# Performance work log

Measured on AMD Instinct MI355X. Metric: run time of the kernel, lower is better.

Reference implementation:

```python
import jax, jax.numpy as jnp
import numpy as np

# dims
C = 16      # input_channels
H = 64      # hidden_channels
HID = 128   # CDEFunc hidden width (hardcoded in source)
OUT = 1     # output_channels
L = 128     # number of time knots -> L-1 spline segments
B = 2048    # batch


def setup_inputs() -> dict:
    key = jax.random.key(0)
    ks = jax.random.split(key, 9)
    n = lambda k, shape, s: (jax.random.normal(k, shape, dtype=jnp.float32) * s)
    return {
        # cubic Hermite spline coeffs: concat(a, b, two_c, three_d) along last dim
        "coeffs": n(ks[0], (B, L - 1, 4 * C), 0.1),
        "W_init": n(ks[1], (H, C), 0.2),
        "b_init": jnp.zeros((H,), jnp.float32),
        "W1": n(ks[2], (HID, H), 0.1),
        "b1": jnp.zeros((HID,), jnp.float32),
        "W2": n(ks[3], (H * C, HID), 0.05),
        "b2": jnp.zeros((H * C,), jnp.float32),
        "W_out": n(ks[4], (OUT, H), 0.1),
        "b_out": jnp.zeros((OUT,), jnp.float32),
    }


def _spline_deriv(coeffs, t):
    """dX/dt of cubic spline at scalar time t. coeffs: (B, L-1, 4C)."""
    idx = jnp.clip(jnp.floor(t).astype(jnp.int32), 0, L - 2)
    seg = jax.lax.dynamic_slice_in_dim(coeffs, idx, 1, axis=1)[:, 0]  # (B, 4C)
    a, b, two_c, three_d = jnp.split(seg, 4, axis=-1)
    fr = t - idx.astype(t.dtype) if hasattr(t, 'dtype') else t - idx
    return b + two_c * fr + three_d * (fr * fr)  # (B, C)


def reference(coeffs, W_init, b_init, W1, b1, W2, b2, W_out, b_out):
    # X(0) = a of first segment (frac = 0)
    X0 = coeffs[:, 0, :C]
    z0 = X0 @ W_init.T + b_init  # (B, H)

    def f(z, dX):
        # CDEFunc: linear-relu-linear-tanh -> (B, H, C), then contract with dX/dt
        h = jax.nn.relu(z @ W1.T + b1)
        g = jnp.tanh(h @ W2.T + b2).reshape(-1, H, C)
        return jnp.einsum('bhc,bc->bh', g, dX)

    dt = jnp.float32(1.0)  # one RK4 step per knot interval

    def step(z, t):
        d0 = _spline_deriv(coeffs, t)
        dm = _spline_deriv(coeffs, t + 0.5 * dt)
        d1 = _spline_deriv(coeffs, t + dt)
        k1 = f(z, d0)
        k2 = f(z + 0.5 * dt * k1, dm)
        k3 = f(z + 0.5 * dt * k2, dm)
        k4 = f(z + dt * k3, d1)
        return z + (dt / 6.0) * (k1 + 2.0 * k2 + 2.0 * k3 + k4), None

    ts = jnp.arange(L - 1, dtype=jnp.float32)
    zT, _ = jax.lax.scan(step, z0, ts)
    return zT @ W_out.T + b_out  # (B, OUT)
```

## Files before the change

kernel.cpp:

```cpp
#include <hip/hip_runtime.h>

#define L_DIM 128
#define BB 8

typedef _Float16 f16;
typedef _Float16 f16x8 __attribute__((ext_vector_type(8)));
typedef float f32x4 __attribute__((ext_vector_type(4)));

__device__ __forceinline__ float fast_tanh_b(float x, float bk) {
    float e = __builtin_amdgcn_exp2f(fmaf(x, 2.8853900817779268f, bk));
    float r = __builtin_amdgcn_rcpf(e + 1.0f);
    return fmaf(-2.0f, r, 1.0f);
}

__attribute__((amdgpu_flat_work_group_size(512, 512), amdgpu_waves_per_eu(2)))
__global__ void
cde_kernel(const float* __restrict__ coeffs,
           const float* __restrict__ W_init, const float* __restrict__ b_init,
           const float* __restrict__ W1, const float* __restrict__ b1,
           const float* __restrict__ W2, const float* __restrict__ b2,
           const float* __restrict__ W_out, const float* __restrict__ b_out,
           float* __restrict__ out)
{
    __shared__ __align__(16) f16   z16[16][72];
    __shared__ __align__(16) f16   h16[16][136];
    __shared__ __align__(16) float dxT[2][3][16][20];
    __shared__ __align__(16) float zf[BB][64];

    const int tid  = threadIdx.x;
    const int blk  = blockIdx.x;
    const int lane = tid & 63;
    const int w    = tid >> 6;
    const int q    = lane >> 4;
    const int lr   = lane & 15;
    const int hh   = w * 8 + (lr & 7);
    const int chp  = lr >> 3;
    const int row0 = (q & 1) * 4 + (q >> 1) * 2;

    f16x8 w2f[8][4];
    float b2k[8];
#pragma unroll
    for (int t8 = 0; t8 < 8; ++t8) {
        const int outc = hh * 16 + 2 * t8 + chp;
        b2k[t8] = 2.8853900817779268f * b2[outc];
#pragma unroll
        for (int kc = 0; kc < 4; ++kc) {
            const float* src = W2 + (size_t)outc * 128 + kc * 32 + q * 8;
            f16x8 v;
#pragma unroll
            for (int i = 0; i < 8; ++i) v[i] = (f16)src[i];
            w2f[t8][kc] = v;
        }
    }
    f16x8 w1f[2];
#pragma unroll
    for (int kc = 0; kc < 2; ++kc) {
        const float* src = W1 + (size_t)(w * 16 + lr) * 64 + kc * 32 + q * 8;
        f16x8 v;
#pragma unroll
        for (int i = 0; i < 8; ++i) v[i] = (f16)src[i];
        w1f[kc] = v;
    }
    const float b1r = b1[w * 16 + lr];
    const f32x4 zero4 = {0.f, 0.f, 0.f, 0.f};

    float z32r[2], ksumr[2];
#pragma unroll
    for (int j = 0; j < 2; ++j) {
        const float* x0 = coeffs + (size_t)(blk * BB + row0 + j) * (L_DIM - 1) * 64;
        float a = b_init[hh];
#pragma unroll
        for (int c = 0; c < 16; ++c) a = fmaf(x0[c], W_init[hh * 16 + c], a);
        z32r[j] = a;
        ksumr[j] = 0.f;
        if (lr < 8) z16[row0 + j][hh] = (f16)a;
    }
    for (int i = tid; i < 8 * 72; i += 512) z16[8 + i / 72][i % 72] = (f16)0.f;
    if (tid < BB * 16) {
        const int b = tid >> 4, c = tid & 15;
        const float* seg = coeffs + (size_t)(blk * BB + b) * (L_DIM - 1) * 64;
        float bv = seg[16 + c], cv = seg[32 + c], dv = seg[48 + c];
        dxT[0][0][c][b] = bv;
        dxT[0][1][c][b] = fmaf(0.25f, dv, fmaf(0.5f, cv, bv));
        dxT[0][2][c][b] = seg[64 + 16 + c];
    }
    __syncthreads();

#define G2TILE(dst, T) \
    f32x4 dst = __builtin_amdgcn_mfma_f32_16x16x32_f16(af0, w2f[T][0], zero4, 0, 0, 0); \
    dst = __builtin_amdgcn_mfma_f32_16x16x32_f16(af1, w2f[T][1], dst, 0, 0, 0);         \
    dst = __builtin_amdgcn_mfma_f32_16x16x32_f16(af2, w2f[T][2], dst, 0, 0, 0);         \
    dst = __builtin_amdgcn_mfma_f32_16x16x32_f16(af3, w2f[T][3], dst, 0, 0, 0);

#define G2TAIL(src, T) {                                                  \
    float u0 = __shfl_xor(src[2], 32);                                    \
    float u1 = __shfl_xor(src[3], 32);                                    \
    float g0 = fast_tanh_b((lane < 32) ? src[0] : u0, b2k[T]);            \
    float g1 = fast_tanh_b((lane < 32) ? src[1] : u1, b2k[T]);            \
    ka0 = fmaf(g0, dvv[(T) & 3].x, ka0);                                  \
    ka1 = fmaf(g1, dvv[(T) & 3].y, ka1); }

    for (int t = 0; t < L_DIM - 1; ++t) {
        const int buf = t & 1;
        float pb = 0.f, pc = 0.f, pd = 0.f, pe = 0.f;
#pragma unroll
        for (int s = 0; s < 4; ++s) {
            {
                f16x8 za0 = *(const f16x8*)&z16[lr][q * 8];
                f16x8 za1 = *(const f16x8*)&z16[lr][32 + q * 8];
                f32x4 hacc = __builtin_amdgcn_mfma_f32_16x16x32_f16(za0, w1f[0], zero4, 0, 0, 0);
                hacc = __builtin_amdgcn_mfma_f32_16x16x32_f16(za1, w1f[1], hacc, 0, 0, 0);
#pragma unroll
                for (int r = 0; r < 4; ++r)
                    h16[q * 4 + r][w * 16 + lr] = (f16)fmaxf(hacc[r] + b1r, 0.f);
            }
            __syncthreads();

            const int ds = (s + 1) >> 1;
            float ka0 = 0.f, ka1 = 0.f;
#pragma unroll
            for (int hf = 0; hf < 2; ++hf) {
                float2 dvv[4];
#pragma unroll
                for (int tt = 0; tt < 4; ++tt)
                    dvv[tt] = *(const float2*)&dxT[buf][ds][2 * (hf * 4 + tt) + chp][row0];
                const f16x8 af0 = *(const f16x8*)&h16[lr][q * 8];
                const f16x8 af1 = *(const f16x8*)&h16[lr][32 + q * 8];
                const f16x8 af2 = *(const f16x8*)&h16[lr][64 + q * 8];
                const f16x8 af3 = *(const f16x8*)&h16[lr][96 + q * 8];
                G2TILE(a0, hf * 4 + 0)
                G2TILE(a1, hf * 4 + 1)
                G2TAIL(a0, hf * 4 + 0)
                G2TILE(a2, hf * 4 + 2)
                G2TAIL(a1, hf * 4 + 1)
                G2TILE(a3, hf * 4 + 3)
                if (hf == 0 && s == 2 && t < L_DIM - 2 && tid < 128) {
                    const int b = tid >> 4, c = tid & 15;
                    const float* seg = coeffs + ((size_t)(blk * BB + b) * (L_DIM - 1) + (t + 1)) * 64;
                    pb = seg[16 + c]; pc = seg[32 + c]; pd = seg[48 + c];
                    pe = (t + 1 < L_DIM - 2) ? seg[80 + c] : 0.f;
                }
                G2TAIL(a2, hf * 4 + 2)
                G2TAIL(a3, hf * 4 + 3)
            }
            ka0 += __shfl_xor(ka0, 8);
            ka1 += __shfl_xor(ka1, 8);
            float zs0, zs1;
            if (s == 3) {
                z32r[0] = fmaf(ksumr[0] + ka0, 1.f / 6.f, z32r[0]); zs0 = z32r[0];
                z32r[1] = fmaf(ksumr[1] + ka1, 1.f / 6.f, z32r[1]); zs1 = z32r[1];
            } else {
                ksumr[0] = (s == 0) ? ka0 : fmaf(2.f, ka0, ksumr[0]);
                ksumr[1] = (s == 0) ? ka1 : fmaf(2.f, ka1, ksumr[1]);
                const float alpha = (s == 2) ? 1.f : 0.5f;
                zs0 = fmaf(alpha, ka0, z32r[0]);
                zs1 = fmaf(alpha, ka1, z32r[1]);
            }
            if (lr < 8) {
                z16[row0 + 0][hh] = (f16)zs0;
                z16[row0 + 1][hh] = (f16)zs1;
            }
            if (s == 3 && t < L_DIM - 2 && tid < 128) {
                const int b = tid >> 4, c = tid & 15;
                dxT[buf ^ 1][0][c][b] = pb;
                dxT[buf ^ 1][1][c][b] = fmaf(0.25f, pd, fmaf(0.5f, pc, pb));
                dxT[buf ^ 1][2][c][b] = (t + 1 < L_DIM - 2) ? pe : (pb + pc + pd);
            }
            __syncthreads();
        }
    }

    if (lr < 8) {
        zf[row0 + 0][hh] = z32r[0];
        zf[row0 + 1][hh] = z32r[1];
    }
    __syncthreads();
    if (tid < 64) {
        const int b = lane >> 3, j0 = lane & 7;
        float p = 0.f;
#pragma unroll
        for (int m = 0; m < 8; ++m) p += zf[b][j0 + 8 * m] * W_out[j0 + 8 * m];
        p += __shfl_xor(p, 1, 64);
        p += __shfl_xor(p, 2, 64);
        p += __shfl_xor(p, 4, 64);
        if (j0 == 0) out[blk * BB + b] = p + b_out[0];
    }
}

extern "C" void kernel_launch(void* const* d_in, const int* in_sizes, int n_in,
                              void* d_out, int out_size, void* d_ws, size_t ws_size,
                              hipStream_t stream) {
    const float* coeffs = (const float*)d_in[0];
    const float* W_init = (const float*)d_in[1];
    const float* b_init = (const float*)d_in[2];
    const float* W1     = (const float*)d_in[3];
    const float* b1     = (const float*)d_in[4];
    const float* W2     = (const float*)d_in[5];
    const float* b2     = (const float*)d_in[6];
    const float* W_out  = (const float*)d_in[7];
    const float* b_out  = (const float*)d_in[8];
    cde_kernel<<<256, 512, 0, stream>>>(coeffs, W_init, b_init, W1, b1, W2, b2,
                                        W_out, b_out, (float*)d_out);
}
```

Before: 662.4 us.

## Preload all spline derivatives into LDS and vectorize hidden-layer store

All spline derivative values for every time step (start and midpoint) are computed and staged into shared memory before the time loop. This replaces the per-step double-buffered global prefetch and its extra writes inside the loop. The first MFMA's operands are swapped so each lane writes four consecutive hidden outputs as one f16x4 store with a float4 bias load, instead of four scalar stores. The cost is about 130KB of LDS per block and a longer prologue.

Result: no change. 666.5 us (+0.6%).

```diff
diff --git a/kernel.cpp b/kernel.cpp
--- a/kernel.cpp
+++ b/kernel.cpp
@@ -4,6 +4,7 @@
 #define BB 8
 
 typedef _Float16 f16;
+typedef _Float16 f16x4 __attribute__((ext_vector_type(4)));
 typedef _Float16 f16x8 __attribute__((ext_vector_type(8)));
 typedef float f32x4 __attribute__((ext_vector_type(4)));
 
@@ -24,8 +25,9 @@
 {
     __shared__ __align__(16) f16   z16[16][72];
     __shared__ __align__(16) f16   h16[16][136];
-    __shared__ __align__(16) float dxT[2][3][16][20];
     __shared__ __align__(16) float zf[BB][64];
+    __shared__ __align__(16) float dxb[128][16][8];
+    __shared__ __align__(16) float dxm[127][16][8];
 
     const int tid  = threadIdx.x;
     const int blk  = blockIdx.x;
@@ -61,7 +63,7 @@
         for (int i = 0; i < 8; ++i) v[i] = (f16)src[i];
         w1f[kc] = v;
     }
-    const float b1r = b1[w * 16 + lr];
+    const float4 b1q = *(const float4*)&b1[w * 16 + q * 4];
     const f32x4 zero4 = {0.f, 0.f, 0.f, 0.f};
 
     float z32r[2], ksumr[2];
@@ -76,22 +78,24 @@
         if (lr < 8) z16[row0 + j][hh] = (f16)a;
     }
     for (int i = tid; i < 8 * 72; i += 512) z16[8 + i / 72][i % 72] = (f16)0.f;
-    if (tid < BB * 16) {
-        const int b = tid >> 4, c = tid & 15;
-        const float* seg = coeffs + (size_t)(blk * BB + b) * (L_DIM - 1) * 64;
-        float bv = seg[16 + c], cv = seg[32 + c], dv = seg[48 + c];
-        dxT[0][0][c][b] = bv;
-        dxT[0][1][c][b] = fmaf(0.25f, dv, fmaf(0.5f, cv, bv));
-        dxT[0][2][c][b] = seg[64 + 16 + c];
+
+#pragma unroll 2
+    for (int i = tid; i < 127 * 128; i += 512) {
+        const int t = i >> 7, j = i & 127;
+        const int c = j & 15, b = (j >> 4) & 7;
+        const float* seg = coeffs + ((size_t)(blk * BB + b) * (L_DIM - 1) + t) * 64;
+        const float bv = seg[16 + c], cv = seg[32 + c], dv = seg[48 + c];
+        dxb[t][c][b] = bv;
+        dxm[t][c][b] = fmaf(0.25f, dv, fmaf(0.5f, cv, bv));
+        if (t == 126) dxb[127][c][b] = bv + cv + dv;
     }
     __syncthreads();
 
-#define G2TILE(dst, T) \
+#define G2T(dst, T) \
     f32x4 dst = __builtin_amdgcn_mfma_f32_16x16x32_f16(af0, w2f[T][0], zero4, 0, 0, 0); \
     dst = __builtin_amdgcn_mfma_f32_16x16x32_f16(af1, w2f[T][1], dst, 0, 0, 0);         \
     dst = __builtin_amdgcn_mfma_f32_16x16x32_f16(af2, w2f[T][2], dst, 0, 0, 0);         \
     dst = __builtin_amdgcn_mfma_f32_16x16x32_f16(af3, w2f[T][3], dst, 0, 0, 0);
-
 #define G2TAIL(src, T) {                                                  \
     float u0 = __shfl_xor(src[2], 32);                                    \
     float u1 = __shfl_xor(src[3], 32);                                    \
@@ -101,45 +105,42 @@
     ka1 = fmaf(g1, dvv[(T) & 3].y, ka1); }
 
     for (int t = 0; t < L_DIM - 1; ++t) {
-        const int buf = t & 1;
-        float pb = 0.f, pc = 0.f, pd = 0.f, pe = 0.f;
 #pragma unroll
         for (int s = 0; s < 4; ++s) {
             {
                 f16x8 za0 = *(const f16x8*)&z16[lr][q * 8];
                 f16x8 za1 = *(const f16x8*)&z16[lr][32 + q * 8];
-                f32x4 hacc = __builtin_amdgcn_mfma_f32_16x16x32_f16(za0, w1f[0], zero4, 0, 0, 0);
-                hacc = __builtin_amdgcn_mfma_f32_16x16x32_f16(za1, w1f[1], hacc, 0, 0, 0);
-#pragma unroll
-                for (int r = 0; r < 4; ++r)
-                    h16[q * 4 + r][w * 16 + lr] = (f16)fmaxf(hacc[r] + b1r, 0.f);
+                f32x4 hacc = __builtin_amdgcn_mfma_f32_16x16x32_f16(w1f[0], za0, zero4, 0, 0, 0);
+                hacc = __builtin_amdgcn_mfma_f32_16x16x32_f16(w1f[1], za1, hacc, 0, 0, 0);
+                f16x4 pp;
+                pp[0] = (f16)fmaxf(hacc[0] + b1q.x, 0.f);
+                pp[1] = (f16)fmaxf(hacc[1] + b1q.y, 0.f);
+                pp[2] = (f16)fmaxf(hacc[2] + b1q.z, 0.f);
+                pp[3] = (f16)fmaxf(hacc[3] + b1q.w, 0.f);
+                *(f16x4*)&h16[lr][w * 16 + q * 4] = pp;
             }
             __syncthreads();
 
-            const int ds = (s + 1) >> 1;
+            const float* dxp = (s == 0) ? &dxb[t][0][0]
+                             : (s == 3) ? &dxb[t + 1][0][0]
+                                        : &dxm[t][0][0];
             float ka0 = 0.f, ka1 = 0.f;
 #pragma unroll
             for (int hf = 0; hf < 2; ++hf) {
                 float2 dvv[4];
 #pragma unroll
                 for (int tt = 0; tt < 4; ++tt)
-                    dvv[tt] = *(const float2*)&dxT[buf][ds][2 * (hf * 4 + tt) + chp][row0];
+                    dvv[tt] = *(const float2*)&dxp[(2 * (hf * 4 + tt) + chp) * 8 + row0];
                 const f16x8 af0 = *(const f16x8*)&h16[lr][q * 8];
                 const f16x8 af1 = *(const f16x8*)&h16[lr][32 + q * 8];
                 const f16x8 af2 = *(const f16x8*)&h16[lr][64 + q * 8];
                 const f16x8 af3 = *(const f16x8*)&h16[lr][96 + q * 8];
-                G2TILE(a0, hf * 4 + 0)
-                G2TILE(a1, hf * 4 + 1)
+                G2T(a0, hf * 4 + 0)
+                G2T(a1, hf * 4 + 1)
                 G2TAIL(a0, hf * 4 + 0)
-                G2TILE(a2, hf * 4 + 2)
+                G2T(a2, hf * 4 + 2)
                 G2TAIL(a1, hf * 4 + 1)
-                G2TILE(a3, hf * 4 + 3)
-                if (hf == 0 && s == 2 && t < L_DIM - 2 && tid < 128) {
-                    const int b = tid >> 4, c = tid & 15;
-                    const float* seg = coeffs + ((size_t)(blk * BB + b) * (L_DIM - 1) + (t + 1)) * 64;
-                    pb = seg[16 + c]; pc = seg[32 + c]; pd = seg[48 + c];
-                    pe = (t + 1 < L_DIM - 2) ? seg[80 + c] : 0.f;
-                }
+                G2T(a3, hf * 4 + 3)
                 G2TAIL(a2, hf * 4 + 2)
                 G2TAIL(a3, hf * 4 + 3)
             }
@@ -159,12 +160,6 @@
             if (lr < 8) {
                 z16[row0 + 0][hh] = (f16)zs0;
                 z16[row0 + 1][hh] = (f16)zs1;
-            }
-            if (s == 3 && t < L_DIM - 2 && tid < 128) {
-                const int b = tid >> 4, c = tid & 15;
-                dxT[buf ^ 1][0][c][b] = pb;
-                dxT[buf ^ 1][1][c][b] = fmaf(0.25f, pd, fmaf(0.5f, pc, pb));
-                dxT[buf ^ 1][2][c][b] = (t + 1 < L_DIM - 2) ? pe : (pb + pc + pd);
             }
             __syncthreads();
         }
```
